# Kernel tuning notes

Measured on AMD Instinct MI355X. Metric: run time of the kernel, lower is better.

## Reference

```python
import jax, jax.numpy as jnp
import numpy as np

# config constants (match init_kwargs)
D_MODEL = 1024        # hidden_size
D_FF = 2048           # intermediate_size
N_EXPERTS = 8         # num_local_experts
TOP_K = 2             # num_experts_per_tok


def setup_inputs() -> dict:
    key = jax.random.key(0)
    k1, k2, k3, k4 = jax.random.split(key, 4)
    layer_input = jax.random.normal(k1, (2, 2048, D_MODEL), dtype=jnp.float32)
    # router: nn.Linear(hidden_size, num_experts, bias=False) -> weight [E, D]
    router_weight = jax.random.normal(k2, (N_EXPERTS, D_MODEL), dtype=jnp.float32) * 0.02
    # ParallelExperts weights: [num_experts, out_features, in_features]
    w_in = jax.random.normal(k3, (N_EXPERTS, 2 * D_FF, D_MODEL), dtype=jnp.float32) * 0.02
    w_out = jax.random.normal(k4, (N_EXPERTS, D_MODEL, D_FF), dtype=jnp.float32) * 0.02
    return {"layer_input": layer_input, "router_weight": router_weight,
            "w_in": w_in, "w_out": w_out}


def _moe_forward(x, router_weight, w_in, w_out):
    # x: [T, D]
    T = x.shape[0]
    logits = x @ router_weight.T                       # [T, E] router logits
    top_vals, top_idx = jax.lax.top_k(logits, TOP_K)   # [T, K]
    gates_k = jax.nn.softmax(top_vals, axis=-1).astype(x.dtype)
    # dense gate matrix: zero for unselected experts -> identical math to
    # the gather / grouped-GEMM / scatter-add path in the torch module.
    gates = jnp.zeros((T, N_EXPERTS), x.dtype).at[
        jnp.arange(T)[:, None], top_idx].set(gates_k)  # [T, E]
    # grouped GEMM #1: [E, T, 2*D_FF]
    h = jnp.einsum('td,efd->etf', x, w_in)
    h1, h2 = jnp.split(h, 2, axis=-1)
    act = jax.nn.silu(h1) * h2                         # SwiGLU: silu(a)*b
    # grouped GEMM #2: [E, T, D]
    y = jnp.einsum('eth,edh->etd', act, w_out)
    # gate-weighted combine (scatter-add equivalent)
    out = jnp.einsum('etd,te->td', y, gates)           # [T, D]
    return out, logits


def reference(layer_input, router_weight, w_in, w_out):
    bsz, length, emb = layer_input.shape
    x = layer_input.reshape(-1, emb)
    out, router_logits = _moe_forward(x, router_weight, w_in, w_out)
    return out.reshape(bsz, length, emb), router_logits
```

## Files before the change

kernel.cpp:

```cpp
#include <hip/hip_runtime.h>
#include <stdint.h>

#define N_TOK   4096
#define DMODEL  1024
#define DFF     2048
#define N_EXP   8
#define N_SLOTS (N_TOK * 2)
#define ROWS_PAD (N_SLOTS + 128)
#define MAX_TILES 72

typedef __bf16 bf16x8 __attribute__((ext_vector_type(8)));
typedef float  f32x4  __attribute__((ext_vector_type(4)));
typedef unsigned short u16;
typedef unsigned short u16x8 __attribute__((ext_vector_type(8)));
typedef unsigned short u16x4 __attribute__((ext_vector_type(4)));

__device__ __forceinline__ u16 f2bf(float f) {
    union { float f; uint32_t u; } v; v.f = f;
    uint32_t r = v.u + 0x7FFFu + ((v.u >> 16) & 1u);
    return (u16)(r >> 16);
}
__device__ __forceinline__ float bf2f(u16 u) {
    union { uint32_t u; float f; } v; v.u = ((uint32_t)u) << 16;
    return v.f;
}

__device__ __forceinline__ void g2l16(const void* gp, void* lp) {
    auto g = reinterpret_cast<const __attribute__((address_space(1))) unsigned int*>(
        reinterpret_cast<uintptr_t>(gp));
    auto l = reinterpret_cast<__attribute__((address_space(3))) unsigned int*>(
        reinterpret_cast<uintptr_t>(lp));
    __builtin_amdgcn_global_load_lds(g, l, 16, 0, 0);
}

__device__ __forceinline__ int idx64(int r, int cb) {
    return r * 64 + ((cb ^ (r & 7)) * 8);
}

#define WIN_V8  (N_EXP * 2 * DFF * DMODEL / 8)
#define WOUT_V8 (N_EXP * DMODEL * DFF / 8)
#define CVT_BLOCKS ((WIN_V8 + WOUT_V8) / 256)
#define RTR_BLOCKS (N_TOK / 4)

__global__ void cvt_router_kernel(const float4* __restrict__ win, const float4* __restrict__ wout,
                                  u16x8* __restrict__ winbf, u16x8* __restrict__ woutbf,
                                  const float* __restrict__ x, const float* __restrict__ rw,
                                  float* __restrict__ logits, int* __restrict__ tok_expert,
                                  float* __restrict__ tok_gate) {
    int bid = blockIdx.x;
    if (bid < CVT_BLOCKS) {
        int i = bid * 256 + threadIdx.x;
        const float4* s; u16x8* d; int k;
        if (i < WIN_V8) { s = win;  d = winbf;  k = i; }
        else            { s = wout; d = woutbf; k = i - WIN_V8; }
        float4 a = s[k * 2];
        float4 b = s[k * 2 + 1];
        u16x8 o = { f2bf(a.x), f2bf(a.y), f2bf(a.z), f2bf(a.w),
                    f2bf(b.x), f2bf(b.y), f2bf(b.z), f2bf(b.w) };
        d[k] = o;
        return;
    }
    int t = (bid - CVT_BLOCKS) * 4 + (threadIdx.x >> 6);
    int lane = threadIdx.x & 63;
    const float* xr = x + (size_t)t * DMODEL;
    float acc[N_EXP];
#pragma unroll
    for (int e = 0; e < N_EXP; ++e) acc[e] = 0.f;
    for (int i = 0; i < DMODEL / 64; ++i) {
        int k = lane + i * 64;
        float xv = xr[k];
#pragma unroll
        for (int e = 0; e < N_EXP; ++e) acc[e] += xv * rw[e * DMODEL + k];
    }
#pragma unroll
    for (int e = 0; e < N_EXP; ++e) {
        float v = acc[e];
        for (int off = 32; off > 0; off >>= 1) v += __shfl_down(v, off, 64);
        acc[e] = v;
    }
    if (lane == 0) {
        float* lg = logits + (size_t)t * N_EXP;
#pragma unroll
        for (int e = 0; e < N_EXP; ++e) lg[e] = acc[e];
        int e0 = 0; float v0 = acc[0];
#pragma unroll
        for (int e = 1; e < N_EXP; ++e) if (acc[e] > v0) { v0 = acc[e]; e0 = e; }
        int e1 = -1; float v1 = -3.0e38f;
#pragma unroll
        for (int e = 0; e < N_EXP; ++e) if (e != e0 && acc[e] > v1) { v1 = acc[e]; e1 = e; }
        float ex = expf(v1 - v0);
        tok_expert[t * 2 + 0] = e0;  tok_gate[t * 2 + 0] = 1.0f / (1.0f + ex);
        tok_expert[t * 2 + 1] = e1;  tok_gate[t * 2 + 1] = ex / (1.0f + ex);
    }
}

__global__ void scan_kernel(const int* __restrict__ tok_expert, int* __restrict__ offs,
                            int* __restrict__ inv, int* __restrict__ tiletab) {
    __shared__ int cnt[N_EXP][257];
    __shared__ int soffs[N_EXP];
    int tid = threadIdx.x;
    int base = tid * 32;
    int loc[N_EXP];
#pragma unroll
    for (int e = 0; e < N_EXP; ++e) loc[e] = 0;
    for (int i = 0; i < 32; ++i) {
        int ex = tok_expert[base + i];
#pragma unroll
        for (int e = 0; e < N_EXP; ++e) loc[e] += (ex == e);
    }
#pragma unroll
    for (int e = 0; e < N_EXP; ++e) cnt[e][tid] = loc[e];
    __syncthreads();
    if (tid < N_EXP) {
        int running = 0;
        for (int t = 0; t < 256; ++t) { int c = cnt[tid][t]; cnt[tid][t] = running; running += c; }
        cnt[tid][256] = running;
    }
    __syncthreads();
    if (tid == 0) {
        int s = 0;
        for (int e = 0; e < N_EXP; ++e) { offs[e] = s; soffs[e] = s; s += cnt[e][256]; }
        offs[N_EXP] = s;
        int n = 0;
        for (int e = 0; e < N_EXP; ++e) {
            int c = cnt[e][256];
            int r0 = soffs[e];
            for (int m = 0; m * 128 < c; ++m) {
                int rem = c - m * 128;
                tiletab[4 + n * 4 + 0] = e;
                tiletab[4 + n * 4 + 1] = r0 + m * 128;
                tiletab[4 + n * 4 + 2] = rem < 128 ? rem : 128;
                ++n;
            }
        }
        tiletab[0] = n;
    }
    __syncthreads();
#pragma unroll
    for (int e = 0; e < N_EXP; ++e) loc[e] = 0;
    for (int i = 0; i < 32; ++i) {
        int ex = tok_expert[base + i];
        int row = 0;
#pragma unroll
        for (int e = 0; e < N_EXP; ++e)
            if (ex == e) { row = soffs[e] + cnt[e][tid] + loc[e]; loc[e]++; }
        inv[base + i] = row;
    }
}

__global__ void gather_kernel(const float* __restrict__ x, const int* __restrict__ inv,
                              u16* __restrict__ Abf) {
    int t = blockIdx.x;
    int r0 = inv[t * 2];
    int r1 = inv[t * 2 + 1];
    float4 v = ((const float4*)(x + (size_t)t * DMODEL))[threadIdx.x];
    u16x4 o = { f2bf(v.x), f2bf(v.y), f2bf(v.z), f2bf(v.w) };
    *(u16x4*)(Abf + (size_t)r0 * DMODEL + threadIdx.x * 4) = o;
    *(u16x4*)(Abf + (size_t)r1 * DMODEL + threadIdx.x * 4) = o;
}

__global__ __launch_bounds__(256, 4)
void gemm1_kernel(const u16* __restrict__ Abf, const u16* __restrict__ winbf,
                  u16* __restrict__ act, const int* __restrict__ tiletab) {
    int bid = blockIdx.x;
    int nt = bid & 31;
    int ti = bid >> 5;
    if (ti >= tiletab[0]) return;
    int e    = tiletab[4 + ti * 4 + 0];
    int row0 = tiletab[4 + ti * 4 + 1];
    int mmax = tiletab[4 + ti * 4 + 2];
    int n0 = nt * 64;
    const u16* wb = winbf + (size_t)e * (2 * DFF) * DMODEL;

    __shared__ u16 lsA[128 * 64];
    __shared__ u16 lsB[2][64 * 64];

    int tid = threadIdx.x, lane = tid & 63, wave = tid >> 6;
    int wm = wave >> 1, wn = wave & 1;
    int s_r8 = lane >> 3;
    int s_cb = ((lane & 7) ^ (lane >> 3)) * 8;

    f32x4 acc[2][4][2];
    f32x4 zero = {0.f, 0.f, 0.f, 0.f};
#pragma unroll
    for (int h = 0; h < 2; ++h)
#pragma unroll
        for (int mi = 0; mi < 4; ++mi)
#pragma unroll
            for (int ni = 0; ni < 2; ++ni) acc[h][mi][ni] = zero;

    for (int kk = 0; kk < DMODEL / 64; ++kk) {
        int k0 = kk * 64;
#pragma unroll
        for (int q = 0; q < 4; ++q) {
            int R0 = wave * 32 + q * 8;
            g2l16(Abf + (size_t)(row0 + R0 + s_r8) * DMODEL + k0 + s_cb, &lsA[R0 * 64]);
        }
#pragma unroll
        for (int h = 0; h < 2; ++h)
#pragma unroll
            for (int q = 0; q < 2; ++q) {
                int R0 = wave * 16 + q * 8;
                g2l16(wb + (size_t)(h * DFF + n0 + R0 + s_r8) * DMODEL + k0 + s_cb,
                      &lsB[h][R0 * 64]);
            }
        __syncthreads();
#pragma unroll
        for (int kh = 0; kh < 2; ++kh) {
            int cb = kh * 4 + (lane >> 4);
            bf16x8 afr[4];
#pragma unroll
            for (int mi = 0; mi < 4; ++mi)
                afr[mi] = *(const bf16x8*)&lsA[idx64(wm * 64 + mi * 16 + (lane & 15), cb)];
#pragma unroll
            for (int h = 0; h < 2; ++h)
#pragma unroll
                for (int ni = 0; ni < 2; ++ni) {
                    bf16x8 bfr = *(const bf16x8*)&lsB[h][idx64(wn * 32 + ni * 16 + (lane & 15), cb)];
#pragma unroll
                    for (int mi = 0; mi < 4; ++mi)
                        acc[h][mi][ni] = __builtin_amdgcn_mfma_f32_16x16x32_bf16(
                            afr[mi], bfr, acc[h][mi][ni], 0, 0, 0);
                }
        }
        __syncthreads();
    }
#pragma unroll
    for (int mi = 0; mi < 4; ++mi)
#pragma unroll
        for (int i = 0; i < 4; ++i) {
            int rl = wm * 64 + mi * 16 + (lane >> 4) * 4 + i;
            if (rl < mmax) {
                size_t rp = (size_t)(row0 + rl) * DFF;
#pragma unroll
                for (int ni = 0; ni < 2; ++ni) {
                    int col = n0 + wn * 32 + ni * 16 + (lane & 15);
                    float a = acc[0][mi][ni][i];
                    float b = acc[1][mi][ni][i];
                    float sv = a / (1.0f + __expf(-a));
                    act[rp + col] = f2bf(sv * b);
                }
            }
        }
}

__global__ __launch_bounds__(256, 4)
void gemm2_kernel(const u16* __restrict__ act, const u16* __restrict__ woutbf,
                  u16* __restrict__ ybA, u16* __restrict__ ybB,
                  const int* __restrict__ tiletab) {
    int bid = blockIdx.x;
    int kc = bid & 1;
    int nt = (bid >> 1) & 7;
    int ti = bid >> 4;
    if (ti >= tiletab[0]) return;
    int e    = tiletab[4 + ti * 4 + 0];
    int row0 = tiletab[4 + ti * 4 + 1];
    int mmax = tiletab[4 + ti * 4 + 2];
    int n0 = nt * 128;
    const u16* wb = woutbf + (size_t)e * DMODEL * DFF;

    __shared__ u16 lsA[128 * 64];
    __shared__ u16 lsB[128 * 64];

    int tid = threadIdx.x, lane = tid & 63, wave = tid >> 6;
    int wm = wave >> 1, wn = wave & 1;
    int s_r8 = lane >> 3;
    int s_cb = ((lane & 7) ^ (lane >> 3)) * 8;
    u16* yb = kc ? ybB : ybA;

    f32x4 acc[4][4];
    f32x4 zero = {0.f, 0.f, 0.f, 0.f};
#pragma unroll
    for (int mi = 0; mi < 4; ++mi)
#pragma unroll
        for (int ni = 0; ni < 4; ++ni) acc[mi][ni] = zero;

    for (int kk = kc * 16; kk < kc * 16 + 16; ++kk) {
        int k0 = kk * 64;
#pragma unroll
        for (int q = 0; q < 4; ++q) {
            int R0 = wave * 32 + q * 8;
            g2l16(act + (size_t)(row0 + R0 + s_r8) * DFF + k0 + s_cb, &lsA[R0 * 64]);
            g2l16(wb + (size_t)(n0 + R0 + s_r8) * DFF + k0 + s_cb, &lsB[R0 * 64]);
        }
        __syncthreads();
#pragma unroll
        for (int kh = 0; kh < 2; ++kh) {
            int cb = kh * 4 + (lane >> 4);
            bf16x8 afr[4];
#pragma unroll
            for (int mi = 0; mi < 4; ++mi)
                afr[mi] = *(const bf16x8*)&lsA[idx64(wm * 64 + mi * 16 + (lane & 15), cb)];
#pragma unroll
            for (int ni = 0; ni < 4; ++ni) {
                bf16x8 bfr = *(const bf16x8*)&lsB[idx64(wn * 64 + ni * 16 + (lane & 15), cb)];
#pragma unroll
                for (int mi = 0; mi < 4; ++mi)
                    acc[mi][ni] = __builtin_amdgcn_mfma_f32_16x16x32_bf16(
                        afr[mi], bfr, acc[mi][ni], 0, 0, 0);
            }
        }
        __syncthreads();
    }
#pragma unroll
    for (int mi = 0; mi < 4; ++mi)
#pragma unroll
        for (int i = 0; i < 4; ++i) {
            int rl = wm * 64 + mi * 16 + (lane >> 4) * 4 + i;
            if (rl < mmax) {
                u16* yrow = yb + (size_t)(row0 + rl) * DMODEL;
#pragma unroll
                for (int ni = 0; ni < 4; ++ni) {
                    int col = n0 + wn * 64 + ni * 16 + (lane & 15);
                    yrow[col] = f2bf(acc[mi][ni][i]);
                }
            }
        }
}

__global__ void combine_kernel(const u16* __restrict__ ybA, const u16* __restrict__ ybB,
                               const int* __restrict__ inv, const float* __restrict__ tok_gate,
                               float* __restrict__ out) {
    int t = blockIdx.x;
    int tid = threadIdx.x;
    __shared__ int sr0, sr1;
    __shared__ float sg0, sg1;
    if (tid == 0) {
        sr0 = inv[t * 2];  sr1 = inv[t * 2 + 1];
        sg0 = tok_gate[t * 2];  sg1 = tok_gate[t * 2 + 1];
    }
    __syncthreads();
    int d = tid * 4;
    u16x4 a0 = *(const u16x4*)(ybA + (size_t)sr0 * DMODEL + d);
    u16x4 b0 = *(const u16x4*)(ybB + (size_t)sr0 * DMODEL + d);
    u16x4 a1 = *(const u16x4*)(ybA + (size_t)sr1 * DMODEL + d);
    u16x4 b1 = *(const u16x4*)(ybB + (size_t)sr1 * DMODEL + d);
    float4 o;
    o.x = sg0 * (bf2f(a0.x) + bf2f(b0.x)) + sg1 * (bf2f(a1.x) + bf2f(b1.x));
    o.y = sg0 * (bf2f(a0.y) + bf2f(b0.y)) + sg1 * (bf2f(a1.y) + bf2f(b1.y));
    o.z = sg0 * (bf2f(a0.z) + bf2f(b0.z)) + sg1 * (bf2f(a1.z) + bf2f(b1.z));
    o.w = sg0 * (bf2f(a0.w) + bf2f(b0.w)) + sg1 * (bf2f(a1.w) + bf2f(b1.w));
    *(float4*)(out + (size_t)t * DMODEL + d) = o;
}

extern "C" void kernel_launch(void* const* d_in, const int* in_sizes, int n_in,
                              void* d_out, int out_size, void* d_ws, size_t ws_size,
                              hipStream_t stream) {
    const float* x    = (const float*)d_in[0];
    const float* rw   = (const float*)d_in[1];
    const float* win  = (const float*)d_in[2];
    const float* wout = (const float*)d_in[3];
    float* out    = (float*)d_out;
    float* logits = out + (size_t)N_TOK * DMODEL;

    char* ws = (char*)d_ws;
    size_t o = 0;
    auto alloc = [&](size_t bytes) -> void* {
        void* p = ws + o;
        o = (o + bytes + 255) & ~(size_t)255;
        return p;
    };
    u16*   Abf      = (u16*)  alloc((size_t)ROWS_PAD * DMODEL * 2);
    u16*   actbuf   = (u16*)  alloc((size_t)ROWS_PAD * DFF * 2);
    u16*   winbf    = (u16*)  alloc((size_t)N_EXP * 2 * DFF * DMODEL * 2);
    u16*   woutbf   = (u16*)  alloc((size_t)N_EXP * DMODEL * DFF * 2);
    int*   offs     = (int*)  alloc(16 * 4);
    int*   inv      = (int*)  alloc(N_SLOTS * 4);
    int*   tok_exp  = (int*)  alloc(N_SLOTS * 4);
    float* tok_gate = (float*)alloc(N_SLOTS * 4);
    int*   tiletab  = (int*)  alloc((4 + MAX_TILES * 4) * 4);
    u16*   ybA      = winbf;
    u16*   ybB      = winbf + (size_t)ROWS_PAD * DMODEL;
    (void)ws_size; (void)in_sizes; (void)n_in; (void)out_size;

    cvt_router_kernel<<<CVT_BLOCKS + RTR_BLOCKS, 256, 0, stream>>>(
        (const float4*)win, (const float4*)wout, (u16x8*)winbf, (u16x8*)woutbf,
        x, rw, logits, tok_exp, tok_gate);
    scan_kernel<<<1, 256, 0, stream>>>(tok_exp, offs, inv, tiletab);
    gather_kernel<<<N_TOK, 256, 0, stream>>>(x, inv, Abf);
    gemm1_kernel<<<MAX_TILES * 32, 256, 0, stream>>>(Abf, winbf, actbuf, tiletab);
    gemm2_kernel<<<MAX_TILES * 16, 256, 0, stream>>>(actbuf, woutbf, ybA, ybB, tiletab);
    combine_kernel<<<N_TOK, 256, 0, stream>>>(ybA, ybB, inv, tok_gate, out);
}
```

Before: 426.1 us.

## Fuse fp32-to-bf16 weight conversion into expert GEMM tile loads

Drops the separate pass that converts all expert weights to bf16. The GEMM kernels now load fp32 weights directly, convert them in registers with packed bf16 conversion instructions, and store them into swizzled LDS. This removes a full write and reread of the converted weights, and yb buffers get their own workspace. In exchange, the inner loops fetch twice the bytes per weight element through registers instead of async global-to-LDS loads, and launch bounds drop to 3 waves per SIMD, which may stall the MFMA loop.

```diff
diff --git a/kernel.cpp b/kernel.cpp
--- a/kernel.cpp
+++ b/kernel.cpp
@@ -12,7 +12,6 @@
 typedef __bf16 bf16x8 __attribute__((ext_vector_type(8)));
 typedef float  f32x4  __attribute__((ext_vector_type(4)));
 typedef unsigned short u16;
-typedef unsigned short u16x8 __attribute__((ext_vector_type(8)));
 typedef unsigned short u16x4 __attribute__((ext_vector_type(4)));
 
 __device__ __forceinline__ u16 f2bf(float f) {
@@ -23,6 +22,13 @@
 __device__ __forceinline__ float bf2f(u16 u) {
     union { uint32_t u; float f; } v; v.u = ((uint32_t)u) << 16;
     return v.f;
+}
+
+__device__ __forceinline__ u16x4 f2bf4(float4 a) {
+    union { uint32_t w[2]; u16x4 o; } u;
+    asm("v_cvt_pk_bf16_f32 %0, %1, %2" : "=v"(u.w[0]) : "v"(a.x), "v"(a.y));
+    asm("v_cvt_pk_bf16_f32 %0, %1, %2" : "=v"(u.w[1]) : "v"(a.z), "v"(a.w));
+    return u.o;
 }
 
 __device__ __forceinline__ void g2l16(const void* gp, void* lp) {
@@ -37,30 +43,12 @@
     return r * 64 + ((cb ^ (r & 7)) * 8);
 }
 
-#define WIN_V8  (N_EXP * 2 * DFF * DMODEL / 8)
-#define WOUT_V8 (N_EXP * DMODEL * DFF / 8)
-#define CVT_BLOCKS ((WIN_V8 + WOUT_V8) / 256)
 #define RTR_BLOCKS (N_TOK / 4)
 
-__global__ void cvt_router_kernel(const float4* __restrict__ win, const float4* __restrict__ wout,
-                                  u16x8* __restrict__ winbf, u16x8* __restrict__ woutbf,
-                                  const float* __restrict__ x, const float* __restrict__ rw,
-                                  float* __restrict__ logits, int* __restrict__ tok_expert,
-                                  float* __restrict__ tok_gate) {
-    int bid = blockIdx.x;
-    if (bid < CVT_BLOCKS) {
-        int i = bid * 256 + threadIdx.x;
-        const float4* s; u16x8* d; int k;
-        if (i < WIN_V8) { s = win;  d = winbf;  k = i; }
-        else            { s = wout; d = woutbf; k = i - WIN_V8; }
-        float4 a = s[k * 2];
-        float4 b = s[k * 2 + 1];
-        u16x8 o = { f2bf(a.x), f2bf(a.y), f2bf(a.z), f2bf(a.w),
-                    f2bf(b.x), f2bf(b.y), f2bf(b.z), f2bf(b.w) };
-        d[k] = o;
-        return;
-    }
-    int t = (bid - CVT_BLOCKS) * 4 + (threadIdx.x >> 6);
+__global__ void router_kernel(const float* __restrict__ x, const float* __restrict__ rw,
+                              float* __restrict__ logits, int* __restrict__ tok_expert,
+                              float* __restrict__ tok_gate) {
+    int t = blockIdx.x * 4 + (threadIdx.x >> 6);
     int lane = threadIdx.x & 63;
     const float* xr = x + (size_t)t * DMODEL;
     float acc[N_EXP];
@@ -159,8 +147,8 @@
     *(u16x4*)(Abf + (size_t)r1 * DMODEL + threadIdx.x * 4) = o;
 }
 
-__global__ __launch_bounds__(256, 4)
-void gemm1_kernel(const u16* __restrict__ Abf, const u16* __restrict__ winbf,
+__global__ __launch_bounds__(256, 3)
+void gemm1_kernel(const u16* __restrict__ Abf, const float* __restrict__ win,
                   u16* __restrict__ act, const int* __restrict__ tiletab) {
     int bid = blockIdx.x;
     int nt = bid & 31;
@@ -170,7 +158,7 @@
     int row0 = tiletab[4 + ti * 4 + 1];
     int mmax = tiletab[4 + ti * 4 + 2];
     int n0 = nt * 64;
-    const u16* wb = winbf + (size_t)e * (2 * DFF) * DMODEL;
+    const float* wsrc = win + (size_t)e * (2 * DFF) * DMODEL;
 
     __shared__ u16 lsA[128 * 64];
     __shared__ u16 lsB[2][64 * 64];
@@ -179,6 +167,10 @@
     int wm = wave >> 1, wn = wave & 1;
     int s_r8 = lane >> 3;
     int s_cb = ((lane & 7) ^ (lane >> 3)) * 8;
+    int lr4 = lane >> 4;
+    int lc  = lane & 15;
+    int cbs = lc >> 1;
+    int hf  = (lane & 1) * 4;
 
     f32x4 acc[2][4][2];
     f32x4 zero = {0.f, 0.f, 0.f, 0.f};
@@ -191,6 +183,13 @@
 
     for (int kk = 0; kk < DMODEL / 64; ++kk) {
         int k0 = kk * 64;
+        float4 v[2][4];
+#pragma unroll
+        for (int h = 0; h < 2; ++h)
+#pragma unroll
+            for (int q2 = 0; q2 < 4; ++q2)
+                v[h][q2] = *(const float4*)(wsrc +
+                    (size_t)(h * DFF + n0 + wave * 16 + q2 * 4 + lr4) * DMODEL + k0 + lc * 4);
 #pragma unroll
         for (int q = 0; q < 4; ++q) {
             int R0 = wave * 32 + q * 8;
@@ -199,10 +198,9 @@
 #pragma unroll
         for (int h = 0; h < 2; ++h)
 #pragma unroll
-            for (int q = 0; q < 2; ++q) {
-                int R0 = wave * 16 + q * 8;
-                g2l16(wb + (size_t)(h * DFF + n0 + R0 + s_r8) * DMODEL + k0 + s_cb,
-                      &lsB[h][R0 * 64]);
+            for (int q2 = 0; q2 < 4; ++q2) {
+                int r = wave * 16 + q2 * 4 + lr4;
+                *(u16x4*)&lsB[h][idx64(r, cbs) + hf] = f2bf4(v[h][q2]);
             }
         __syncthreads();
 #pragma unroll
@@ -244,8 +242,8 @@
         }
 }
 
-__global__ __launch_bounds__(256, 4)
-void gemm2_kernel(const u16* __restrict__ act, const u16* __restrict__ woutbf,
+__global__ __launch_bounds__(256, 3)
+void gemm2_kernel(const u16* __restrict__ act, const float* __restrict__ wout,
                   u16* __restrict__ ybA, u16* __restrict__ ybB,
                   const int* __restrict__ tiletab) {
     int bid = blockIdx.x;
@@ -257,7 +255,7 @@
     int row0 = tiletab[4 + ti * 4 + 1];
     int mmax = tiletab[4 + ti * 4 + 2];
     int n0 = nt * 128;
-    const u16* wb = woutbf + (size_t)e * DMODEL * DFF;
+    const float* wsrc = wout + (size_t)e * DMODEL * DFF;
 
     __shared__ u16 lsA[128 * 64];
     __shared__ u16 lsB[128 * 64];
@@ -266,6 +264,10 @@
     int wm = wave >> 1, wn = wave & 1;
     int s_r8 = lane >> 3;
     int s_cb = ((lane & 7) ^ (lane >> 3)) * 8;
+    int lr4 = lane >> 4;
+    int lc  = lane & 15;
+    int cbs = lc >> 1;
+    int hf  = (lane & 1) * 4;
     u16* yb = kc ? ybB : ybA;
 
     f32x4 acc[4][4];
@@ -278,10 +280,24 @@
     for (int kk = kc * 16; kk < kc * 16 + 16; ++kk) {
         int k0 = kk * 64;
 #pragma unroll
-        for (int q = 0; q < 4; ++q) {
-            int R0 = wave * 32 + q * 8;
-            g2l16(act + (size_t)(row0 + R0 + s_r8) * DFF + k0 + s_cb, &lsA[R0 * 64]);
-            g2l16(wb + (size_t)(n0 + R0 + s_r8) * DFF + k0 + s_cb, &lsB[R0 * 64]);
+        for (int g = 0; g < 2; ++g) {
+            float4 v[4];
+#pragma unroll
+            for (int q2 = 0; q2 < 4; ++q2)
+                v[q2] = *(const float4*)(wsrc +
+                    (size_t)(n0 + wave * 32 + g * 16 + q2 * 4 + lr4) * DFF + k0 + lc * 4);
+            if (g == 0) {
+#pragma unroll
+                for (int q = 0; q < 4; ++q) {
+                    int R0 = wave * 32 + q * 8;
+                    g2l16(act + (size_t)(row0 + R0 + s_r8) * DFF + k0 + s_cb, &lsA[R0 * 64]);
+                }
+            }
+#pragma unroll
+            for (int q2 = 0; q2 < 4; ++q2) {
+                int r = wave * 32 + g * 16 + q2 * 4 + lr4;
+                *(u16x4*)&lsB[idx64(r, cbs) + hf] = f2bf4(v[q2]);
+            }
         }
         __syncthreads();
 #pragma unroll
@@ -362,23 +378,19 @@
     };
     u16*   Abf      = (u16*)  alloc((size_t)ROWS_PAD * DMODEL * 2);
     u16*   actbuf   = (u16*)  alloc((size_t)ROWS_PAD * DFF * 2);
-    u16*   winbf    = (u16*)  alloc((size_t)N_EXP * 2 * DFF * DMODEL * 2);
-    u16*   woutbf   = (u16*)  alloc((size_t)N_EXP * DMODEL * DFF * 2);
+    u16*   ybA      = (u16*)  alloc((size_t)ROWS_PAD * DMODEL * 2);
+    u16*   ybB      = (u16*)  alloc((size_t)ROWS_PAD * DMODEL * 2);
     int*   offs     = (int*)  alloc(16 * 4);
     int*   inv      = (int*)  alloc(N_SLOTS * 4);
     int*   tok_exp  = (int*)  alloc(N_SLOTS * 4);
     float* tok_gate = (float*)alloc(N_SLOTS * 4);
     int*   tiletab  = (int*)  alloc((4 + MAX_TILES * 4) * 4);
-    u16*   ybA      = winbf;
-    u16*   ybB      = winbf + (size_t)ROWS_PAD * DMODEL;
     (void)ws_size; (void)in_sizes; (void)n_in; (void)out_size;
 
-    cvt_router_kernel<<<CVT_BLOCKS + RTR_BLOCKS, 256, 0, stream>>>(
-        (const float4*)win, (const float4*)wout, (u16x8*)winbf, (u16x8*)woutbf,
-        x, rw, logits, tok_exp, tok_gate);
+    router_kernel<<<RTR_BLOCKS, 256, 0, stream>>>(x, rw, logits, tok_exp, tok_gate);
     scan_kernel<<<1, 256, 0, stream>>>(tok_exp, offs, inv, tiletab);
     gather_kernel<<<N_TOK, 256, 0, stream>>>(x, inv, Abf);
-    gemm1_kernel<<<MAX_TILES * 32, 256, 0, stream>>>(Abf, winbf, actbuf, tiletab);
-    gemm2_kernel<<<MAX_TILES * 16, 256, 0, stream>>>(actbuf, woutbf, ybA, ybB, tiletab);
+    gemm1_kernel<<<MAX_TILES * 32, 256, 0, stream>>>(Abf, win, actbuf, tiletab);
+    gemm2_kernel<<<MAX_TILES * 16, 256, 0, stream>>>(actbuf, wout, ybA, ybB, tiletab);
     combine_kernel<<<N_TOK, 256, 0, stream>>>(ybA, ybB, inv, tok_gate, out);
 }
```

After: 502.9 us. +18.0%, slower.
